# Performance work log

Measured on AMD Instinct MI355X. Metric: run time of the kernel, lower is better.

## Reference

```python
import jax, jax.numpy as jnp
import numpy as np

B, N, F_IN = 32, 1024, 128
DIM, NUM_HEAD = 16, 8
D = DIM * NUM_HEAD  # 128


def setup_inputs() -> dict:
    key = jax.random.key(0)
    ks = jax.random.split(key, 8)
    atom_query = jax.random.normal(ks[0], (B, N, F_IN), dtype=jnp.float32)
    mask = (jax.random.uniform(ks[1], (B, N, 1)) < 0.9).astype(jnp.float32)
    s = 1.0 / np.sqrt(F_IN)
    Wq = jax.random.normal(ks[2], (F_IN, D), dtype=jnp.float32) * s
    bq = jnp.zeros((D,), dtype=jnp.float32)
    Wk = jax.random.normal(ks[3], (F_IN, D), dtype=jnp.float32) * s
    bk = jnp.zeros((D,), dtype=jnp.float32)
    Wv = jax.random.normal(ks[4], (F_IN, D), dtype=jnp.float32) * s
    bv = jnp.zeros((D,), dtype=jnp.float32)
    return {"atom_query": atom_query, "mask": mask,
            "Wq": Wq, "bq": bq, "Wk": Wk, "bk": bk, "Wv": Wv, "bv": bv}


def reference(atom_query, mask, Wq, bq, Wk, bk, Wv, bv):
    scale = 0.5  # self.scale
    q = atom_query @ Wq + bq            # [B, N, D]
    k = atom_query @ Wk + bk            # [B, N, D]
    v = atom_query @ Wv + bv            # [B, N, D] (v_proj=True)
    dk = jnp.asarray(q.shape[-1], jnp.float32) ** (-scale)
    q = q * dk
    energy = jnp.einsum('bqd,bkd->bqk', q, k)      # [B, N, N]
    energy = mask * energy                          # mask broadcasts over k
    agg = jnp.sum(energy, axis=-1, keepdims=True)   # [B, N, 1]
    agg = mask * agg
    # norm=False branch skipped
    agg = agg + (1.0 - mask) * (-1e9)
    attn = jax.nn.softmax(agg, axis=1)              # softmax over query axis
    context = jnp.sum(mask * (attn * v), axis=1)    # [B, D]
    return attn, context
```

## Files before the change

kernel.cpp:

```cpp
#include <hip/hip_runtime.h>

#define B    32
#define N    1024
#define FIN  128
#define CHN  16
#define ROWS 64
#define GRID (B * CHN)

#define OFF_PASUM 64
#define OFF_U     (OFF_PASUM + B*CHN*FIN)
#define OFF_C     (OFF_U + B*FIN)
#define OFF_P     (OFF_C + B)
#define OFF_WPART (OFF_P + B*N)
#define OFF_M     (OFF_WPART + B*CHN*FIN)
#define OFF_L     (OFF_M + B*CHN)
#define OFF_S     (OFF_L + B*CHN)

__device__ __forceinline__ float aload(const float* p) {
    return __hip_atomic_load(p, __ATOMIC_RELAXED, __HIP_MEMORY_SCOPE_AGENT);
}
__device__ __forceinline__ void astore(float* p, float v) {
    __hip_atomic_store(p, v, __ATOMIC_RELAXED, __HIP_MEMORY_SCOPE_AGENT);
}

__global__ __launch_bounds__(256) void k_pass1(
    const float* __restrict__ aq,
    const float* __restrict__ Wq, const float* __restrict__ bq,
    const float* __restrict__ Wk, const float* __restrict__ bk,
    float* __restrict__ ws)
{
    const int b = blockIdx.x >> 4, ch = blockIdx.x & 15;
    const int tid = threadIdx.x;
    int* cnt = (int*)ws;

    const float4* g4 = (const float4*)aq + ((size_t)b * N + ch * ROWS) * 32;
    float4 acc = make_float4(0.f, 0.f, 0.f, 0.f);
    #pragma unroll
    for (int i = 0; i < 8; ++i) {
        float4 v = g4[i * 256 + tid];
        acc.x += v.x; acc.y += v.y; acc.z += v.z; acc.w += v.w;
    }
    __shared__ float4 sh4[256];
    __shared__ int flag;
    sh4[tid] = acc;
    __syncthreads();
    if (tid < 32) {
        float4 r = sh4[tid];
        #pragma unroll
        for (int g = 1; g < 8; ++g) {
            float4 t = sh4[g * 32 + tid];
            r.x += t.x; r.y += t.y; r.z += t.z; r.w += t.w;
        }
        float* dst = ws + OFF_PASUM + (b * CHN + ch) * FIN + tid * 4;
        astore(dst + 0, r.x); astore(dst + 1, r.y);
        astore(dst + 2, r.z); astore(dst + 3, r.w);
    }
    __syncthreads();
    if (tid == 0) {
        __threadfence();
        int old = atomicAdd(&cnt[b], 1);
        flag = (old == CHN - 1);
    }
    __syncthreads();
    if (!flag) return;

    __threadfence();
    __shared__ float asum_s[FIN], ksum_s[FIN];
    __shared__ float red[256];
    const int f = tid & 127, h = tid >> 7;
    if (tid < FIN) {
        float a = 0.f;
        #pragma unroll
        for (int c = 0; c < CHN; ++c)
            a += aload(ws + OFF_PASUM + (b * CHN + c) * FIN + f);
        asum_s[f] = a;
    }
    __syncthreads();
    {
        float ks = 0.f;
        #pragma unroll 8
        for (int i = 0; i < 64; ++i) {
            int fi = h * 64 + i;
            ks += asum_s[fi] * Wk[fi * FIN + f];
        }
        red[tid] = ks;
    }
    __syncthreads();
    if (tid < FIN) ksum_s[f] = red[f] + red[f + 128] + 1024.f * bk[f];
    __syncthreads();
    {
        float uu = 0.f;
        #pragma unroll 8
        for (int i = 0; i < 64; ++i) {
            int d = h * 64 + i;
            uu += Wq[f * FIN + d] * ksum_s[d];
        }
        red[tid] = uu;
    }
    __syncthreads();
    if (tid < FIN) ws[OFF_U + b * FIN + f] = red[f] + red[f + 128];
    if (tid < 64) {
        float cc = bq[tid] * ksum_s[tid] + bq[tid + 64] * ksum_s[tid + 64];
        #pragma unroll
        for (int off = 32; off > 0; off >>= 1) cc += __shfl_xor(cc, off);
        if (tid == 0) ws[OFF_C + b] = cc;
    }
}

__global__ __launch_bounds__(256) void k_main(
    const float* __restrict__ aq, const float* __restrict__ mask,
    const float* __restrict__ Wv, const float* __restrict__ bv,
    float* __restrict__ ws, float* __restrict__ out)
{
    const int b = blockIdx.x >> 4, ch = blockIdx.x & 15;
    const int tid = threadIdx.x, f = tid & 127, h = tid >> 7;
    int* cnt = (int*)ws;

    __shared__ float tile[ROWS * FIN];
    __shared__ float red[256];
    __shared__ float u_s[FIN], mp_s[ROWS];
    __shared__ float c_sh;
    __shared__ int flag;

    {
        const float4* g4 = (const float4*)aq + ((size_t)b * N + ch * ROWS) * 32;
        float4* t4 = (float4*)tile;
        #pragma unroll
        for (int i = 0; i < 8; ++i) {
            int g = i * 256 + tid, row = g >> 5, c4 = g & 31;
            t4[row * 32 + (c4 ^ (row & 31))] = g4[g];
        }
    }
    if (tid < FIN) u_s[f] = ws[OFF_U + b * FIN + f];
    if (tid == 0) c_sh = ws[OFF_C + b];
    __syncthreads();

    {
        const int r = tid & 63, q = tid >> 6;
        const float4* t4 = (const float4*)tile;
        const float4* u4 = (const float4*)u_s;
        float acc = 0.f;
        #pragma unroll
        for (int jj = 0; jj < 8; ++jj) {
            int j = q * 8 + jj;
            float4 a = t4[r * 32 + (j ^ (r & 31))];
            float4 uu = u4[j];
            acc += a.x * uu.x + a.y * uu.y + a.z * uu.z + a.w * uu.w;
        }
        red[tid] = acc;
    }
    __syncthreads();
    if (tid < ROWS) {
        const float dkc = 0.08838834764831845f;
        float dot = red[tid] + red[tid + 64] + red[tid + 128] + red[tid + 192];
        float m = mask[b * N + ch * ROWS + tid];
        float aggv = m * (dkc * (dot + c_sh)) + (1.f - m) * (-1e9f);
        float Mc = aggv;
        #pragma unroll
        for (int off = 32; off > 0; off >>= 1) Mc = fmaxf(Mc, __shfl_xor(Mc, off));
        float p = __expf(aggv - Mc);
        float mp = m * p;
        astore(ws + OFF_P + b * N + ch * ROWS + tid, p);
        mp_s[tid] = mp;
        float Lc = p, Sc = mp;
        #pragma unroll
        for (int off = 32; off > 0; off >>= 1) {
            Lc += __shfl_xor(Lc, off);
            Sc += __shfl_xor(Sc, off);
        }
        if (tid == 0) {
            astore(ws + OFF_M + b * CHN + ch, Mc);
            astore(ws + OFF_L + b * CHN + ch, Lc);
            astore(ws + OFF_S + b * CHN + ch, Sc);
        }
    }
    __syncthreads();
    {
        float w = 0.f;
        #pragma unroll 8
        for (int i = 0; i < 32; ++i) {
            int r = h * 32 + i;
            w += mp_s[r] * tile[r * FIN + ((((f >> 2) ^ (r & 31)) << 2) | (f & 3))];
        }
        red[tid] = w;
    }
    __syncthreads();
    if (tid < FIN) astore(ws + OFF_WPART + (b * CHN + ch) * FIN + f, red[f] + red[f + 128]);
    __syncthreads();
    if (tid == 0) {
        __threadfence();
        int old = atomicAdd(&cnt[B + b], 1);
        flag = (old == CHN - 1);
    }
    __syncthreads();
    if (!flag) return;

    __threadfence();
    float M = -3.0e38f;
    #pragma unroll
    for (int c = 0; c < CHN; ++c) M = fmaxf(M, aload(ws + OFF_M + b * CHN + c));
    float Em[CHN], L = 0.f, S = 0.f;
    #pragma unroll
    for (int c = 0; c < CHN; ++c) {
        float e = __expf(aload(ws + OFF_M + b * CHN + c) - M);
        Em[c] = e;
        L += e * aload(ws + OFF_L + b * CHN + c);
        S += e * aload(ws + OFF_S + b * CHN + c);
    }
    const float invL = 1.f / L;
    #pragma unroll
    for (int j = 0; j < 4; ++j) {
        int n = j * 256 + tid;
        out[b * N + n] = aload(ws + OFF_P + b * N + n) * Em[j * 4 + (tid >> 6)] * invL;
    }
    if (tid < FIN) {
        float w = 0.f;
        #pragma unroll
        for (int c = 0; c < CHN; ++c)
            w += Em[c] * aload(ws + OFF_WPART + (b * CHN + c) * FIN + f);
        u_s[f] = w;
    }
    __syncthreads();
    {
        float ctx = 0.f;
        #pragma unroll 8
        for (int i = 0; i < 64; ++i) {
            int fi = h * 64 + i;
            ctx += u_s[fi] * Wv[fi * FIN + f];
        }
        red[tid] = ctx;
    }
    __syncthreads();
    if (tid < FIN)
        out[B * N + b * FIN + f] = (red[f] + red[f + 128]) * invL + S * invL * bv[f];
}

extern "C" void kernel_launch(void* const* d_in, const int* in_sizes, int n_in,
                              void* d_out, int out_size, void* d_ws, size_t ws_size,
                              hipStream_t stream) {
    const float* aq   = (const float*)d_in[0];
    const float* mask = (const float*)d_in[1];
    const float* Wq   = (const float*)d_in[2];
    const float* bq   = (const float*)d_in[3];
    const float* Wk   = (const float*)d_in[4];
    const float* bk   = (const float*)d_in[5];
    const float* Wv   = (const float*)d_in[6];
    const float* bv   = (const float*)d_in[7];
    float* ws  = (float*)d_ws;
    float* out = (float*)d_out;

    hipMemsetAsync(ws, 0, 2 * B * sizeof(int), stream);
    k_pass1<<<GRID, 256, 0, stream>>>(aq, Wq, bq, Wk, bk, ws);
    k_main <<<GRID, 256, 0, stream>>>(aq, mask, Wv, bv, ws, out);
}
```

Measured before the change: 121.2 us.

## Fuse two kernels into one with per-batch spin barrier and register staging

Merges the column-sum/projection kernel and the main attention kernel into a single launch. Each block loads its atom tile once into registers, publishes partial column sums, then spin-waits on a per-batch counter until all 16 chunk blocks arrive. After that, every block redundantly computes the Wk/Wq projection vector itself instead of reading it from a second kernel. This removes one launch and one reread of the input. In exchange it relies on all 512 blocks being co-resident, which risks deadlock, and it repeats the small projection work in every block. Cross-chunk reductions are also split across both halves of the block.

New measurement: 171.9 us. +41.8%, slower.

```diff
diff --git a/kernel.cpp b/kernel.cpp
--- a/kernel.cpp
+++ b/kernel.cpp
@@ -8,9 +8,7 @@
 #define GRID (B * CHN)
 
 #define OFF_PASUM 64
-#define OFF_U     (OFF_PASUM + B*CHN*FIN)
-#define OFF_C     (OFF_U + B*FIN)
-#define OFF_P     (OFF_C + B)
+#define OFF_P     (OFF_PASUM + B*CHN*FIN)
 #define OFF_WPART (OFF_P + B*N)
 #define OFF_M     (OFF_WPART + B*CHN*FIN)
 #define OFF_L     (OFF_M + B*CHN)
@@ -23,92 +21,10 @@
     __hip_atomic_store(p, v, __ATOMIC_RELAXED, __HIP_MEMORY_SCOPE_AGENT);
 }
 
-__global__ __launch_bounds__(256) void k_pass1(
-    const float* __restrict__ aq,
+__global__ __launch_bounds__(256) void k_one(
+    const float* __restrict__ aq, const float* __restrict__ mask,
     const float* __restrict__ Wq, const float* __restrict__ bq,
     const float* __restrict__ Wk, const float* __restrict__ bk,
-    float* __restrict__ ws)
-{
-    const int b = blockIdx.x >> 4, ch = blockIdx.x & 15;
-    const int tid = threadIdx.x;
-    int* cnt = (int*)ws;
-
-    const float4* g4 = (const float4*)aq + ((size_t)b * N + ch * ROWS) * 32;
-    float4 acc = make_float4(0.f, 0.f, 0.f, 0.f);
-    #pragma unroll
-    for (int i = 0; i < 8; ++i) {
-        float4 v = g4[i * 256 + tid];
-        acc.x += v.x; acc.y += v.y; acc.z += v.z; acc.w += v.w;
-    }
-    __shared__ float4 sh4[256];
-    __shared__ int flag;
-    sh4[tid] = acc;
-    __syncthreads();
-    if (tid < 32) {
-        float4 r = sh4[tid];
-        #pragma unroll
-        for (int g = 1; g < 8; ++g) {
-            float4 t = sh4[g * 32 + tid];
-            r.x += t.x; r.y += t.y; r.z += t.z; r.w += t.w;
-        }
-        float* dst = ws + OFF_PASUM + (b * CHN + ch) * FIN + tid * 4;
-        astore(dst + 0, r.x); astore(dst + 1, r.y);
-        astore(dst + 2, r.z); astore(dst + 3, r.w);
-    }
-    __syncthreads();
-    if (tid == 0) {
-        __threadfence();
-        int old = atomicAdd(&cnt[b], 1);
-        flag = (old == CHN - 1);
-    }
-    __syncthreads();
-    if (!flag) return;
-
-    __threadfence();
-    __shared__ float asum_s[FIN], ksum_s[FIN];
-    __shared__ float red[256];
-    const int f = tid & 127, h = tid >> 7;
-    if (tid < FIN) {
-        float a = 0.f;
-        #pragma unroll
-        for (int c = 0; c < CHN; ++c)
-            a += aload(ws + OFF_PASUM + (b * CHN + c) * FIN + f);
-        asum_s[f] = a;
-    }
-    __syncthreads();
-    {
-        float ks = 0.f;
-        #pragma unroll 8
-        for (int i = 0; i < 64; ++i) {
-            int fi = h * 64 + i;
-            ks += asum_s[fi] * Wk[fi * FIN + f];
-        }
-        red[tid] = ks;
-    }
-    __syncthreads();
-    if (tid < FIN) ksum_s[f] = red[f] + red[f + 128] + 1024.f * bk[f];
-    __syncthreads();
-    {
-        float uu = 0.f;
-        #pragma unroll 8
-        for (int i = 0; i < 64; ++i) {
-            int d = h * 64 + i;
-            uu += Wq[f * FIN + d] * ksum_s[d];
-        }
-        red[tid] = uu;
-    }
-    __syncthreads();
-    if (tid < FIN) ws[OFF_U + b * FIN + f] = red[f] + red[f + 128];
-    if (tid < 64) {
-        float cc = bq[tid] * ksum_s[tid] + bq[tid + 64] * ksum_s[tid + 64];
-        #pragma unroll
-        for (int off = 32; off > 0; off >>= 1) cc += __shfl_xor(cc, off);
-        if (tid == 0) ws[OFF_C + b] = cc;
-    }
-}
-
-__global__ __launch_bounds__(256) void k_main(
-    const float* __restrict__ aq, const float* __restrict__ mask,
     const float* __restrict__ Wv, const float* __restrict__ bv,
     float* __restrict__ ws, float* __restrict__ out)
 {
@@ -118,21 +34,93 @@
 
     __shared__ float tile[ROWS * FIN];
     __shared__ float red[256];
-    __shared__ float u_s[FIN], mp_s[ROWS];
+    __shared__ float asum_s[FIN], ksum_s[FIN], u_s[FIN], mp_s[ROWS];
     __shared__ float c_sh;
     __shared__ int flag;
 
-    {
-        const float4* g4 = (const float4*)aq + ((size_t)b * N + ch * ROWS) * 32;
+    float4 stage[8];
+    const float4* g4 = (const float4*)aq + ((size_t)b * N + ch * ROWS) * 32;
+    #pragma unroll
+    for (int i = 0; i < 8; ++i) stage[i] = g4[i * 256 + tid];
+
+    float4 cs = stage[0];
+    #pragma unroll
+    for (int i = 1; i < 8; ++i) {
+        cs.x += stage[i].x; cs.y += stage[i].y; cs.z += stage[i].z; cs.w += stage[i].w;
+    }
+    {
+        float4* t4s = (float4*)tile;
+        t4s[tid] = cs;
+        __syncthreads();
+        if (tid < 32) {
+            float4 r = t4s[tid];
+            #pragma unroll
+            for (int g = 1; g < 8; ++g) {
+                float4 t = t4s[g * 32 + tid];
+                r.x += t.x; r.y += t.y; r.z += t.z; r.w += t.w;
+            }
+            float* dst = ws + OFF_PASUM + (b * CHN + ch) * FIN + tid * 4;
+            astore(dst + 0, r.x); astore(dst + 1, r.y);
+            astore(dst + 2, r.z); astore(dst + 3, r.w);
+        }
+        __syncthreads();
+    }
+    {
         float4* t4 = (float4*)tile;
         #pragma unroll
         for (int i = 0; i < 8; ++i) {
             int g = i * 256 + tid, row = g >> 5, c4 = g & 31;
-            t4[row * 32 + (c4 ^ (row & 31))] = g4[g];
-        }
-    }
-    if (tid < FIN) u_s[f] = ws[OFF_U + b * FIN + f];
-    if (tid == 0) c_sh = ws[OFF_C + b];
+            t4[row * 32 + (c4 ^ (row & 31))] = stage[i];
+        }
+    }
+    if (tid == 0) {
+        __threadfence();
+        atomicAdd(&cnt[b], 1);
+        while (__hip_atomic_load(&cnt[b], __ATOMIC_ACQUIRE,
+                                 __HIP_MEMORY_SCOPE_AGENT) < CHN) {}
+    }
+    __syncthreads();
+    __threadfence();
+
+    {
+        float a = 0.f;
+        #pragma unroll
+        for (int c = 0; c < 8; ++c)
+            a += aload(ws + OFF_PASUM + (b * CHN + h * 8 + c) * FIN + f);
+        red[tid] = a;
+    }
+    __syncthreads();
+    if (tid < FIN) asum_s[f] = red[f] + red[f + 128];
+    __syncthreads();
+    {
+        float ks = 0.f;
+        #pragma unroll 8
+        for (int i = 0; i < 64; ++i) {
+            int fi = h * 64 + i;
+            ks += asum_s[fi] * Wk[fi * FIN + f];
+        }
+        red[tid] = ks;
+    }
+    __syncthreads();
+    if (tid < FIN) ksum_s[f] = red[f] + red[f + 128] + 1024.f * bk[f];
+    __syncthreads();
+    {
+        float uu = 0.f;
+        #pragma unroll 8
+        for (int i = 0; i < 64; ++i) {
+            int d = h * 64 + i;
+            uu += Wq[f * FIN + d] * ksum_s[d];
+        }
+        red[tid] = uu;
+    }
+    __syncthreads();
+    if (tid < FIN) u_s[f] = red[f] + red[f + 128];
+    if (tid < 64) {
+        float cc = bq[tid] * ksum_s[tid] + bq[tid + 64] * ksum_s[tid + 64];
+        #pragma unroll
+        for (int off = 32; off > 0; off >>= 1) cc += __shfl_xor(cc, off);
+        if (tid == 0) c_sh = cc;
+    }
     __syncthreads();
 
     {
@@ -185,7 +173,8 @@
         red[tid] = w;
     }
     __syncthreads();
-    if (tid < FIN) astore(ws + OFF_WPART + (b * CHN + ch) * FIN + f, red[f] + red[f + 128]);
+    if (tid < FIN)
+        astore(ws + OFF_WPART + (b * CHN + ch) * FIN + f, red[f] + red[f + 128]);
     __syncthreads();
     if (tid == 0) {
         __threadfence();
@@ -213,13 +202,15 @@
         int n = j * 256 + tid;
         out[b * N + n] = aload(ws + OFF_P + b * N + n) * Em[j * 4 + (tid >> 6)] * invL;
     }
-    if (tid < FIN) {
+    {
         float w = 0.f;
         #pragma unroll
-        for (int c = 0; c < CHN; ++c)
-            w += Em[c] * aload(ws + OFF_WPART + (b * CHN + c) * FIN + f);
-        u_s[f] = w;
-    }
+        for (int c = 0; c < 8; ++c)
+            w += Em[h * 8 + c] * aload(ws + OFF_WPART + (b * CHN + h * 8 + c) * FIN + f);
+        red[tid] = w;
+    }
+    __syncthreads();
+    if (tid < FIN) u_s[f] = red[f] + red[f + 128];
     __syncthreads();
     {
         float ctx = 0.f;
@@ -249,7 +240,6 @@
     float* ws  = (float*)d_ws;
     float* out = (float*)d_out;
 
-    hipMemsetAsync(ws, 0, 2 * B * sizeof(int), stream);
-    k_pass1<<<GRID, 256, 0, stream>>>(aq, Wq, bq, Wk, bk, ws);
-    k_main <<<GRID, 256, 0, stream>>>(aq, mask, Wv, bv, ws, out);
-}
+    hipMemsetAsync(ws, 0, 64 * sizeof(int), stream);
+    k_one<<<GRID, 256, 0, stream>>>(aq, mask, Wq, bq, Wk, bk, Wv, bv, ws, out);
+}
```
